# Kernel tuning notes

Measured on AMD Instinct MI355X. Metric: run time of the kernel, lower is better.

## Reference

```python
import jax, jax.numpy as jnp
import numpy as np

GELU = lambda v: jax.nn.gelu(v, approximate=False)  # torch nn.GELU default (exact erf)


def _gconv(x, w):
    # grouped conv1d, valid padding; w: (C,1,K), groups=C. lax conv = cross-correlation, same as torch.
    return jax.lax.conv_general_dilated(x, w, (1,), [(0, 0)],
                                        dimension_numbers=('NCH', 'OIH', 'NCH'),
                                        feature_group_count=x.shape[1])


def _conv(x, w, b):
    # dense conv1d, kernel 3, padding=1
    y = jax.lax.conv_general_dilated(x, w, (1,), [(1, 1)],
                                     dimension_numbers=('NCH', 'OIH', 'NCH'))
    return y + b[None, :, None]


def setup_inputs() -> dict:
    key = jax.random.key(0)
    ks = jax.random.split(key, 12)
    B, C, L = 8, 64, 2048
    H, FL, HD, TD, level = 32, 8, 64, 16, 3
    Cs = (1 + level) * C  # 256 channels into the ODE
    n = lambda k, s: (jax.random.normal(k, s) * 0.05).astype(jnp.float32)
    z = lambda s: jnp.zeros(s, jnp.float32)
    return dict(
        x=jax.random.normal(ks[0], (B, C, L), jnp.float32),
        # DyWAN_QR params
        sw1=n(ks[1], (H, C)), sb1=z((H,)),
        sw2=n(ks[2], (H, H)), sb2=z((H,)),
        sw3=n(ks[3], (2 * FL, H)), sb3=z((2 * FL,)),
        # ODE time embed / FiLM params
        tw1=n(ks[4], (TD, 1)), tb1=z((TD,)),
        tw2=n(ks[5], (TD, TD)), tb2=z((TD,)),
        cw=n(ks[6], (2 * HD, TD)), cb=z((2 * HD,)),
        # ODE conv stack params
        k1=n(ks[7], (HD, Cs, 3)), kb1=z((HD,)),
        k2=n(ks[8], (HD, HD, 3)), kb2=z((HD,)),
        k3=n(ks[9], (Cs, HD, 3)), kb3=z((Cs,)),
    )


def reference(x, sw1, sb1, sw2, sb2, sw3, sb3, tw1, tb1, tw2, tb2, cw, cb,
              k1, kb1, k2, kb2, k3, kb3):
    B, C, L = x.shape
    level, FL, T = 3, 8, 5

    def dywan(a):
        # stat_net: adaptive max pool over L -> (B,C) -> Linear -> GELU
        feat = GELU(jnp.max(a, axis=-1) @ sw1.T + sb1)
        raw = GELU(feat @ sw2.T + sb2) @ sw3.T + sb3  # (B, 2*FL)
        lo_raw, hi_raw = raw[:, :FL], raw[:, FL:]
        # QR of an (FL,1) column vector == L2 normalization (up to LAPACK sign)
        lo = lo_raw / jnp.linalg.norm(lo_raw, axis=1, keepdims=True)
        hi = hi_raw / jnp.linalg.norm(hi_raw, axis=1, keepdims=True)
        return lo, hi

    pad = FL - 1
    coeffs = [x]
    approx = x
    for _ in range(level):
        lo, hi = dywan(approx)
        lo_f = jnp.broadcast_to(lo.mean(0)[None, None, :], (C, 1, FL))
        hi_f = jnp.broadcast_to(hi.mean(0)[None, None, :], (C, 1, FL))
        ap = jnp.pad(approx, ((0, 0), (0, 0), (pad // 2, pad - pad // 2)), mode='reflect')
        new_approx = _gconv(ap, lo_f)[..., :L]
        coeffs.append(_gconv(ap, hi_f)[..., :L])
        approx = new_approx
    stacked = jnp.concatenate(coeffs, axis=1)  # (B, (1+level)*C, L)

    def ode_f(t, y):
        te = jnp.reshape(t, (1, 1)).astype(y.dtype)
        te = GELU(te @ tw1.T + tb1) @ tw2.T + tb2          # (1, TD)
        cond = te @ cw.T + cb                               # (1, 2*HD)
        hd = cond.shape[1] // 2
        gamma, beta = cond[:, :hd], cond[:, hd:]
        h = _conv(y, k1, kb1)
        h = (1.0 + gamma[:, :, None]) * h + beta[:, :, None]  # FiLM
        h = GELU(h)
        h = GELU(_conv(h, k2, kb2))
        return _conv(h, k3, kb3)

    # dopri5 tableau, fixed grid over linspace(0, 1, T) (b7 = 0, so 6 stages)
    hs = 1.0 / (T - 1)
    y = stacked
    for i in range(T - 1):
        t0 = i * hs
        s1 = ode_f(t0, y)
        s2 = ode_f(t0 + hs / 5, y + hs * (1 / 5) * s1)
        s3 = ode_f(t0 + 3 * hs / 10, y + hs * (3 / 40 * s1 + 9 / 40 * s2))
        s4 = ode_f(t0 + 4 * hs / 5, y + hs * (44 / 45 * s1 - 56 / 15 * s2 + 32 / 9 * s3))
        s5 = ode_f(t0 + 8 * hs / 9, y + hs * (19372 / 6561 * s1 - 25360 / 2187 * s2
                                              + 64448 / 6561 * s3 - 212 / 729 * s4))
        s6 = ode_f(t0 + hs, y + hs * (9017 / 3168 * s1 - 355 / 33 * s2 + 46732 / 5247 * s3
                                      + 49 / 176 * s4 - 5103 / 18656 * s5))
        y = y + hs * (35 / 384 * s1 + 500 / 1113 * s3 + 125 / 192 * s4
                      - 2187 / 6784 * s5 + 11 / 84 * s6)
    ode_out = y

    yl = ode_out[:, :C, :]
    yh0 = ode_out[:, C:2 * C, :]
    yh1 = ode_out[:, 2 * C:3 * C, :]
    yh2 = ode_out[:, 3 * C:4 * C, :]

    dx = ode_f(jnp.float32(1.0), ode_out)
    inner = jnp.sum(stacked * dx, axis=(1, 2))  # (B,)
    ecloss = jnp.mean(inner ** 2)
    return (yl, yh0, yh1, yh2, ecloss)
```

## Files before the change

kernel.cpp:

```cpp
#include <hip/hip_runtime.h>
#include <math.h>

#define B 8
#define C 64
#define L 2048
#define CS 256
#define BCL  (B*C*L)
#define BCSL (B*CS*L)
#define HS 0.25f

typedef unsigned short u16;
typedef unsigned int   u32;
typedef __attribute__((ext_vector_type(8))) short sh8;
typedef __attribute__((ext_vector_type(4))) float f4;
typedef __attribute__((ext_vector_type(8))) unsigned short us8;
typedef __attribute__((ext_vector_type(4))) unsigned short us4;

__device__ __forceinline__ float gelu(float x) {
    return 0.5f * x * (1.0f + erff(x * 0.70710678118654752440f));
}
__device__ __forceinline__ u16 f2b(float f) {
    u32 u = __float_as_uint(f);
    u32 r = u + 0x7FFFu + ((u >> 16) & 1u);
    return (u16)(r >> 16);
}
__device__ __forceinline__ float b2f(u16 h) {
    return __uint_as_float(((u32)h) << 16);
}

struct ComboB { const u16* p[6]; float c[6]; };

__global__ __launch_bounds__(256) void prep_k(const float* __restrict__ w,
        u16* __restrict__ dst, int IC, int OC) {
    int idx = blockIdx.x * 256 + threadIdx.x;
    int OCG = OC >> 4;
    int j = idx & 7, lane = (idx >> 3) & 63, t = idx >> 9;
    int ocg = t % OCG, c = t / OCG;
    int oc = ocg * 16 + (lane & 15);
    int K = c * 32 + ((lane >> 4) & 3) * 8 + j;
    int kk = K / IC, ic = K % IC;
    dst[idx] = f2b(w[((size_t)oc * IC + ic) * 3 + kk]);
}

__global__ void cond25_k(const float* __restrict__ tw1, const float* __restrict__ tb1,
                         const float* __restrict__ tw2, const float* __restrict__ tb2,
                         const float* __restrict__ cw, const float* __restrict__ cb,
                         float* __restrict__ condall) {
    __shared__ float te1[16], te2[16];
    int tix = blockIdx.x;
    int tid = threadIdx.x;
    double add[6] = {0.0, 0.25/5.0, 3.0*0.25/10.0, 4.0*0.25/5.0, 8.0*0.25/9.0, 0.25};
    float t = (tix == 24) ? 1.0f : (float)((double)(tix / 6) * 0.25 + add[tix % 6]);
    if (tid < 16) te1[tid] = gelu(t * tw1[tid] + tb1[tid]);
    __syncthreads();
    if (tid < 16) {
        float s = tb2[tid];
        for (int k = 0; k < 16; ++k) s += te1[k] * tw2[tid*16+k];
        te2[tid] = s;
    }
    __syncthreads();
    float s = cb[tid];
    for (int j = 0; j < 16; ++j) s += te2[j] * cw[tid*16+j];
    condall[tix*128 + tid] = s;
}

template<int NC, int EPI>
__global__ __launch_bounds__(256, 8) void fused_k(ComboB in,
        const u16* __restrict__ wp1, const float* __restrict__ kb1,
        const u16* __restrict__ wp2, const float* __restrict__ kb2,
        const u16* __restrict__ wp3, const float* __restrict__ kb3,
        const float* __restrict__ condall, int tix,
        u16* __restrict__ outSb,
        float* __restrict__ ytr, u16* __restrict__ yb,
        float* __restrict__ outp, const float* __restrict__ stacked,
        double* __restrict__ inner)
{
    __shared__ u16 xs1[16][264];
    __shared__ u16 h1t[12][72];
    __shared__ u16 h2t[10][72];
    __shared__ u16 ypart[8][264];
    __shared__ double sred[4];
    const int tid = threadIdx.x;
    const int bx  = blockIdx.x;
    const int tile = ((bx & 7) << 5) | (bx >> 3);
    const int l0  = tile * 8;
    const int b   = blockIdx.y;

    const float cy1 = HS*(35.f/384.f), cy3 = HS*(500.f/1113.f),
                cy4 = HS*(125.f/192.f), cy5 = -HS*(2187.f/6784.f),
                cy6 = HS*(11.f/84.f);

    for (int i = tid; i < 264; i += 256) ((u32*)&xs1[14][0])[i] = 0;

    #pragma unroll
    for (int it = 0; it < 2; ++it) {
        int idx = it * 256 + tid;
        if (idx < 448) {
            int r = idx >> 5, c8 = idx & 31;
            int gl = l0 - 3 + r;
            us8 val;
            if (gl >= 0 && gl < L) {
                size_t a = ((size_t)b * L + gl) * 256 + c8 * 8;
                us8 v0 = *(const us8*)(in.p[0] + a);
                if (NC == 1) {
                    val = v0;
                } else {
                    float f[8], yp[8];
                    #pragma unroll
                    for (int j = 0; j < 8; ++j) { f[j] = b2f(v0[j]); yp[j] = 0.f; }
                    #pragma unroll
                    for (int t = 1; t < NC; ++t) {
                        us8 vt = *(const us8*)(in.p[t] + a);
                        #pragma unroll
                        for (int j = 0; j < 8; ++j) {
                            float bv = b2f(vt[j]);
                            f[j] += in.c[t] * bv;
                            if ((EPI == 1 || EPI == 2) && (t == 1 || t == 3 || t == 4 || t == 5)) {
                                float cy = (t == 1) ? cy1 : (t == 3) ? cy3 : (t == 4) ? cy4 : cy5;
                                yp[j] += cy * bv;
                            }
                        }
                    }
                    #pragma unroll
                    for (int j = 0; j < 8; ++j) val[j] = f2b(f[j]);
                    if ((EPI == 1 || EPI == 2) && r >= 3 && r < 11) {
                        us8 ypk;
                        #pragma unroll
                        for (int j = 0; j < 8; ++j) ypk[j] = f2b(yp[j]);
                        *(us8*)&ypart[r - 3][c8 * 8] = ypk;
                    }
                }
            } else {
                #pragma unroll
                for (int j = 0; j < 8; ++j) val[j] = 0;
            }
            *(us8*)&xs1[r][c8 * 8] = val;
        }
    }
    __syncthreads();

    const int wave = tid >> 6, lane = tid & 63;
    const int nlo = lane & 15, quad = lane >> 4;

    f4 a1 = {0.f,0.f,0.f,0.f};
    {
        const sh8* w1 = (const sh8*)wp1;
        for (int c = 0; c < 24; ++c) {
            int kk = c >> 3, ic0 = (c & 7) << 5;
            sh8 A = w1[(c*4 + wave)*64 + lane];
            int row = nlo + kk; row = row > 15 ? 15 : row;
            sh8 Bv = *(const sh8*)&xs1[row][ic0 + quad*8];
            a1 = __builtin_amdgcn_mfma_f32_16x16x32_bf16(A, Bv, a1, 0, 0, 0);
        }
    }
    {
        const float* cd = condall + tix*128;
        int p = nlo;
        int gp = l0 - 2 + p;
        bool ok = (gp >= 0) && (gp < L);
        if (p < 12) {
            #pragma unroll
            for (int reg = 0; reg < 4; ++reg) {
                int oc = wave*16 + quad*4 + reg;
                float v = (1.f + cd[oc]) * (a1[reg] + kb1[oc]) + cd[64+oc];
                h1t[p][oc] = ok ? f2b(gelu(v)) : (u16)0;
            }
        }
    }
    __syncthreads();

    f4 a2 = {0.f,0.f,0.f,0.f};
    {
        const sh8* w2 = (const sh8*)wp2;
        #pragma unroll
        for (int c = 0; c < 6; ++c) {
            int kk = c >> 1, ic0 = (c & 1) << 5;
            sh8 A = w2[(c*4 + wave)*64 + lane];
            int row = nlo + kk; row = row > 11 ? 11 : row;
            sh8 Bv = *(const sh8*)&h1t[row][ic0 + quad*8];
            a2 = __builtin_amdgcn_mfma_f32_16x16x32_bf16(A, Bv, a2, 0, 0, 0);
        }
    }
    {
        int q = nlo;
        int gq = l0 - 1 + q;
        bool ok = (gq >= 0) && (gq < L);
        if (q < 10) {
            #pragma unroll
            for (int reg = 0; reg < 4; ++reg) {
                int oc = wave*16 + quad*4 + reg;
                h2t[q][oc] = ok ? f2b(gelu(a2[reg] + kb2[oc])) : (u16)0;
            }
        }
    }
    __syncthreads();

    f4 a3[4];
    #pragma unroll
    for (int mf = 0; mf < 4; ++mf) a3[mf] = f4{0.f,0.f,0.f,0.f};
    {
        const sh8* w3 = (const sh8*)wp3;
        #pragma unroll
        for (int c = 0; c < 6; ++c) {
            int kk = c >> 1, ic0 = (c & 1) << 5;
            int row = nlo + kk; row = row > 9 ? 9 : row;
            sh8 B0 = *(const sh8*)&h2t[row][ic0 + quad*8];
            #pragma unroll
            for (int mf = 0; mf < 4; ++mf) {
                sh8 A = w3[(c*16 + wave*4 + mf)*64 + lane];
                a3[mf] = __builtin_amdgcn_mfma_f32_16x16x32_bf16(A, B0, a3[mf], 0, 0, 0);
            }
        }
    }

    const int pos = l0 + nlo;
    if (EPI == 3) {
        double acc = 0.0;
        if (nlo < 8) {
            #pragma unroll
            for (int mf = 0; mf < 4; ++mf)
                #pragma unroll
                for (int reg = 0; reg < 4; ++reg) {
                    int oc = (wave*4 + mf)*16 + quad*4 + reg;
                    size_t idx = ((size_t)b*CS + oc)*L + pos;
                    float dx = a3[mf][reg] + kb3[oc];
                    acc += (double)stacked[idx] * (double)dx;
                }
        }
        #pragma unroll
        for (int off = 32; off > 0; off >>= 1) acc += __shfl_down(acc, off, 64);
        if (lane == 0) sred[wave] = acc;
        __syncthreads();
        if (tid == 0) atomicAdd(&inner[b], sred[0] + sred[1] + sred[2] + sred[3]);
    } else if (EPI == 0) {
        if (nlo < 8) {
            #pragma unroll
            for (int mf = 0; mf < 4; ++mf) {
                int baseoc = (wave*4 + mf)*16 + quad*4;
                us4 pk;
                #pragma unroll
                for (int reg = 0; reg < 4; ++reg)
                    pk[reg] = f2b(a3[mf][reg] + kb3[baseoc + reg]);
                *(us4*)(outSb + ((size_t)b*L + pos)*256 + baseoc) = pk;
            }
        }
    } else {
        if (nlo < 8) {
            #pragma unroll
            for (int mf = 0; mf < 4; ++mf) {
                int baseoc = (wave*4 + mf)*16 + quad*4;
                size_t ta = ((size_t)b*L + pos)*256 + baseoc;
                us4 yp4 = *(const us4*)&ypart[nlo][baseoc];
                f4 y4 = *(const f4*)(ytr + ta);
                us4 pk;
                f4 yo;
                #pragma unroll
                for (int reg = 0; reg < 4; ++reg) {
                    int oc = baseoc + reg;
                    float s6 = a3[mf][reg] + kb3[oc];
                    float yv = y4[reg] + b2f(yp4[reg]) + cy6 * s6;
                    yo[reg] = yv;
                    pk[reg] = f2b(yv);
                    if (EPI == 2) {
                        size_t oidx = (((size_t)(oc >> 6)*B + b)*64 + (oc & 63))*L + pos;
                        outp[oidx] = yv;
                    }
                }
                if (EPI == 1) *(f4*)(ytr + ta) = yo;
                *(us4*)(yb + ta) = pk;
            }
        }
    }
}

__global__ __launch_bounds__(256) void rowmax_k(const float* __restrict__ a, float* __restrict__ bm) {
    __shared__ float red[256];
    int row = blockIdx.x;
    const float* p = a + (size_t)row * L;
    float m = -1e30f;
    for (int t = threadIdx.x; t < L; t += 256) m = fmaxf(m, p[t]);
    red[threadIdx.x] = m;
    __syncthreads();
    for (int s = 128; s > 0; s >>= 1) {
        if (threadIdx.x < s) red[threadIdx.x] = fmaxf(red[threadIdx.x], red[threadIdx.x + s]);
        __syncthreads();
    }
    if (threadIdx.x == 0) bm[row] = red[0];
}

__global__ __launch_bounds__(256) void mlp_k(const float* __restrict__ bm,
    const float* __restrict__ sw1, const float* __restrict__ sb1,
    const float* __restrict__ sw2, const float* __restrict__ sb2,
    const float* __restrict__ sw3, const float* __restrict__ sb3,
    float* __restrict__ filt) {
    __shared__ float m[8][64], f1[8][32], f2[8][32], raw[8][16], nrm[8][2];
    int tid = threadIdx.x;
    for (int i = tid; i < 512; i += 256) m[i >> 6][i & 63] = bm[i];
    __syncthreads();
    {
        int b = tid >> 5, h = tid & 31;
        float s = sb1[h];
        for (int c = 0; c < 64; ++c) s += m[b][c] * sw1[h*64+c];
        f1[b][h] = gelu(s);
    }
    __syncthreads();
    {
        int b = tid >> 5, h = tid & 31;
        float s = sb2[h];
        for (int k = 0; k < 32; ++k) s += f1[b][k] * sw2[h*32+k];
        f2[b][h] = gelu(s);
    }
    __syncthreads();
    if (tid < 128) {
        int b = tid >> 4, j = tid & 15;
        float s = sb3[j];
        for (int k = 0; k < 32; ++k) s += f2[b][k] * sw3[j*32+k];
        raw[b][j] = s;
    }
    __syncthreads();
    if (tid < 16) {
        int b = tid >> 1, half = tid & 1;
        float s = 0.f;
        for (int j = 0; j < 8; ++j) { float v = raw[b][half*8+j]; s += v*v; }
        nrm[b][half] = sqrtf(s);
    }
    __syncthreads();
    if (tid < 16) {
        int half = tid >> 3;
        float s = 0.f;
        for (int b = 0; b < 8; ++b) s += raw[b][tid] / nrm[b][half];
        filt[tid] = s * 0.125f;
    }
}

__global__ __launch_bounds__(256) void wconv_k(const float* __restrict__ ap,
    const float* __restrict__ filt, float* __restrict__ apOut,
    float* __restrict__ stacked, int lev) {
    __shared__ float f[16];
    if (threadIdx.x < 16) f[threadIdx.x] = filt[threadIdx.x];
    __syncthreads();
    size_t idx = (size_t)blockIdx.x * 256 + threadIdx.x;
    int l = (int)(idx & 2047);
    size_t bc = idx >> 11;
    int c = (int)(bc & 63), b = (int)(bc >> 6);
    const float* row = ap + (bc << 11);
    float lo = 0.f, hi = 0.f;
    #pragma unroll
    for (int k = 0; k < 8; ++k) {
        int mI = l + k - 3;
        mI = mI < 0 ? -mI : (mI >= L ? 2*L - 2 - mI : mI);
        float v = row[mI];
        lo += v * f[k];
        hi += v * f[8+k];
    }
    apOut[idx] = lo;
    stacked[((size_t)b * CS + (size_t)(lev+1) * 64 + c) * L + l] = hi;
}

__global__ __launch_bounds__(256) void copyx_k(const float* __restrict__ x, float* __restrict__ st) {
    size_t i = (size_t)blockIdx.x * 256 + threadIdx.x;
    size_t b = i >> 17, rem = i & 131071;
    st[b * ((size_t)CS*L) + rem] = x[i];
}

__global__ __launch_bounds__(256) void tinit_k(const float* __restrict__ st,
        float* __restrict__ ytr, u16* __restrict__ yb) {
    __shared__ float t[64][65];
    const int tid = threadIdx.x;
    const int l0 = blockIdx.x * 64, c0 = blockIdx.y * 64, b = blockIdx.z;
    #pragma unroll
    for (int k = 0; k < 16; ++k) {
        int c = k * 4 + (tid >> 6), l = tid & 63;
        t[c][l] = st[((size_t)b*CS + c0 + c) * L + l0 + l];
    }
    __syncthreads();
    #pragma unroll
    for (int k = 0; k < 16; ++k) {
        int p = k * 4 + (tid >> 6), ch = tid & 63;
        float v = t[ch][p];
        size_t ta = ((size_t)b * L + l0 + p) * 256 + c0 + ch;
        ytr[ta] = v;
        yb[ta] = f2b(v);
    }
}

__global__ void ecfin_k(const double* __restrict__ inner, float* __restrict__ out) {
    double s = 0.0;
    for (int b = 0; b < 8; ++b) s += inner[b] * inner[b];
    out[BCSL] = (float)(s / 8.0);
}

extern "C" void kernel_launch(void* const* d_in, const int* in_sizes, int n_in,
                              void* d_out, int out_size, void* d_ws, size_t ws_size,
                              hipStream_t stream) {
    const float* x   = (const float*)d_in[0];
    const float* sw1 = (const float*)d_in[1];
    const float* sb1 = (const float*)d_in[2];
    const float* sw2 = (const float*)d_in[3];
    const float* sb2 = (const float*)d_in[4];
    const float* sw3 = (const float*)d_in[5];
    const float* sb3 = (const float*)d_in[6];
    const float* tw1 = (const float*)d_in[7];
    const float* tb1 = (const float*)d_in[8];
    const float* tw2 = (const float*)d_in[9];
    const float* tb2 = (const float*)d_in[10];
    const float* cw  = (const float*)d_in[11];
    const float* cb  = (const float*)d_in[12];
    const float* k1  = (const float*)d_in[13];
    const float* kb1 = (const float*)d_in[14];
    const float* k2  = (const float*)d_in[15];
    const float* kb2 = (const float*)d_in[16];
    const float* k3  = (const float*)d_in[17];
    const float* kb3 = (const float*)d_in[18];
    float* out = (float*)d_out;

    char* cur = (char*)d_ws;
    auto alloc = [&](size_t bytes) { void* p = cur; cur += (bytes + 255) & ~(size_t)255; return p; };
    float* stacked = (float*)alloc(BCSL * 4);
    float* ytr     = (float*)alloc(BCSL * 4);
    u16*   yb      = (u16*)  alloc(BCSL * 2);
    u16*   sbuf[5];
    for (int i = 0; i < 5; ++i) sbuf[i] = (u16*)alloc(BCSL * 2);
    float* cond  = (float*)alloc(3200 * 4);
    float* bmax  = (float*)alloc(512 * 4);
    float* filt  = (float*)alloc(16 * 4);
    double* inner = (double*)alloc(8 * 8);
    u16* wp1 = (u16*)alloc(49152 * 2);
    u16* wp2 = (u16*)alloc(12288 * 2);
    u16* wp3 = (u16*)alloc(49152 * 2);

    u16 *s1b = sbuf[0], *s2b = sbuf[1], *s3b = sbuf[2], *s4b = sbuf[3], *s5b = sbuf[4];

    hipMemsetAsync(inner, 0, 8 * sizeof(double), stream);

    prep_k<<<192, 256, 0, stream>>>(k1, wp1, CS, C);
    prep_k<<<48,  256, 0, stream>>>(k2, wp2, C,  C);
    prep_k<<<192, 256, 0, stream>>>(k3, wp3, C,  CS);
    cond25_k<<<25, 128, 0, stream>>>(tw1, tb1, tw2, tb2, cw, cb, cond);

    copyx_k<<<4096, 256, 0, stream>>>(x, stacked);
    const float* apIn = x;
    float* apBuf[2] = {(float*)s1b, (float*)s2b};
    for (int lev = 0; lev < 3; ++lev) {
        rowmax_k<<<512, 256, 0, stream>>>(apIn, bmax);
        mlp_k<<<1, 256, 0, stream>>>(bmax, sw1, sb1, sw2, sb2, sw3, sb3, filt);
        float* apOut = apBuf[lev & 1];
        wconv_k<<<4096, 256, 0, stream>>>(apIn, filt, apOut, stacked, lev);
        apIn = apOut;
    }
    tinit_k<<<dim3(32, 4, 8), 256, 0, stream>>>(stacked, ytr, yb);

    const float hs = HS;
    dim3 cg(256, 8);
    #define LAUNCH(NC, EPI, CIN, TIX, OUTSB, OUTP, STK) \
        fused_k<NC, EPI><<<cg, 256, 0, stream>>>(CIN, wp1, kb1, wp2, kb2, wp3, kb3, \
            cond, TIX, OUTSB, ytr, yb, OUTP, STK, inner)

    for (int i = 0; i < 4; ++i) {
        ComboB cA{}; cA.p[0] = yb;
        LAUNCH(1, 0, cA, i*6+0, s1b, nullptr, nullptr);

        ComboB cB{}; cB.p[0] = yb; cB.p[1] = s1b; cB.c[1] = hs*(1.f/5.f);
        LAUNCH(2, 0, cB, i*6+1, s2b, nullptr, nullptr);

        ComboB cC{}; cC.p[0] = yb;
        cC.p[1] = s1b; cC.c[1] = hs*(3.f/40.f);
        cC.p[2] = s2b; cC.c[2] = hs*(9.f/40.f);
        LAUNCH(3, 0, cC, i*6+2, s3b, nullptr, nullptr);

        ComboB cD{}; cD.p[0] = yb;
        cD.p[1] = s1b; cD.c[1] = hs*(44.f/45.f);
        cD.p[2] = s2b; cD.c[2] = -hs*(56.f/15.f);
        cD.p[3] = s3b; cD.c[3] = hs*(32.f/9.f);
        LAUNCH(4, 0, cD, i*6+3, s4b, nullptr, nullptr);

        ComboB cE{}; cE.p[0] = yb;
        cE.p[1] = s1b; cE.c[1] = hs*(19372.f/6561.f);
        cE.p[2] = s2b; cE.c[2] = -hs*(25360.f/2187.f);
        cE.p[3] = s3b; cE.c[3] = hs*(64448.f/6561.f);
        cE.p[4] = s4b; cE.c[4] = -hs*(212.f/729.f);
        LAUNCH(5, 0, cE, i*6+4, s5b, nullptr, nullptr);

        ComboB cF{}; cF.p[0] = yb;
        cF.p[1] = s1b; cF.c[1] = hs*(9017.f/3168.f);
        cF.p[2] = s2b; cF.c[2] = -hs*(355.f/33.f);
        cF.p[3] = s3b; cF.c[3] = hs*(46732.f/5247.f);
        cF.p[4] = s4b; cF.c[4] = hs*(49.f/176.f);
        cF.p[5] = s5b; cF.c[5] = -hs*(5103.f/18656.f);
        if (i < 3) {
            LAUNCH(6, 1, cF, i*6+5, nullptr, nullptr, nullptr);
        } else {
            LAUNCH(6, 2, cF, i*6+5, nullptr, out, nullptr);
        }
    }

    ComboB cZ{}; cZ.p[0] = yb;
    LAUNCH(1, 3, cZ, 24, nullptr, nullptr, stacked);
    ecfin_k<<<1, 1, 0, stream>>>(inner, out);
    #undef LAUNCH
}
```

Baseline: 782.1 us.

## Fuse all six RK stages into one kernel per step with LDS halo recompute

Replaces the 24 per-stage kernel launches with 4 per-step kernels. Each workgroup loads a 16-position tile plus an 18-position halo of y into LDS, then computes all six Dormand-Prince stages locally, keeping the intermediate stage results in shared memory instead of global bf16 buffers. This removes the global round-trips for s1..s5 and most launch overhead, at the cost of redundant halo compute (52 rows for 16 outputs), large LDS use (~1 workgroup per CU) and fewer blocks. The final dx/ecloss evaluation moves to a separate 16-wide kernel.

Measured after the change: 1.235 ms. +57.9%, slower.

```diff
diff --git a/kernel.cpp b/kernel.cpp
--- a/kernel.cpp
+++ b/kernel.cpp
@@ -27,8 +27,6 @@
 __device__ __forceinline__ float b2f(u16 h) {
     return __uint_as_float(((u32)h) << 16);
 }
-
-struct ComboB { const u16* p[6]; float c[6]; };
 
 __global__ __launch_bounds__(256) void prep_k(const float* __restrict__ w,
         u16* __restrict__ dst, int IC, int OC) {
@@ -64,212 +62,397 @@
     condall[tix*128 + tid] = s;
 }
 
-template<int NC, int EPI>
-__global__ __launch_bounds__(256, 8) void fused_k(ComboB in,
-        const u16* __restrict__ wp1, const float* __restrict__ kb1,
-        const u16* __restrict__ wp2, const float* __restrict__ kb2,
-        const u16* __restrict__ wp3, const float* __restrict__ kb3,
-        const float* __restrict__ condall, int tix,
-        u16* __restrict__ outSb,
-        float* __restrict__ ytr, u16* __restrict__ yb,
-        float* __restrict__ outp, const float* __restrict__ stacked,
-        double* __restrict__ inner)
+
+template<int K, int STEP>
+__device__ __forceinline__ void do_stage(int tid, int l0, int b,
+    const u16* __restrict__ wp1, const float* __restrict__ kb1,
+    const u16* __restrict__ wp2, const float* __restrict__ kb2,
+    const u16* __restrict__ wp3, const float* __restrict__ kb3,
+    const float* __restrict__ condall,
+    u16 (&ybt)[52][264], u16 (&xs)[52][264],
+    u16 (&s1t)[46][264], u16 (&s2t)[40][264], u16 (&s3t)[34][264],
+    u16 (&s4t)[28][264], u16 (&s5t)[22][264],
+    u16 (&h1)[52][72], u16 (&h2)[52][72],
+    float* __restrict__ ytr, u16* __restrict__ ybo, float* __restrict__ outp)
 {
-    __shared__ u16 xs1[16][264];
-    __shared__ u16 h1t[12][72];
-    __shared__ u16 h2t[10][72];
-    __shared__ u16 ypart[8][264];
-    __shared__ double sred[4];
-    const int tid = threadIdx.x;
-    const int bx  = blockIdx.x;
-    const int tile = ((bx & 7) << 5) | (bx >> 3);
-    const int l0  = tile * 8;
-    const int b   = blockIdx.y;
-
-    const float cy1 = HS*(35.f/384.f), cy3 = HS*(500.f/1113.f),
-                cy4 = HS*(125.f/192.f), cy5 = -HS*(2187.f/6784.f),
-                cy6 = HS*(11.f/84.f);
-
-    for (int i = tid; i < 264; i += 256) ((u32*)&xs1[14][0])[i] = 0;
-
-    #pragma unroll
-    for (int it = 0; it < 2; ++it) {
-        int idx = it * 256 + tid;
-        if (idx < 448) {
-            int r = idx >> 5, c8 = idx & 31;
-            int gl = l0 - 3 + r;
-            us8 val;
-            if (gl >= 0 && gl < L) {
-                size_t a = ((size_t)b * L + gl) * 256 + c8 * 8;
-                us8 v0 = *(const us8*)(in.p[0] + a);
-                if (NC == 1) {
-                    val = v0;
-                } else {
-                    float f[8], yp[8];
-                    #pragma unroll
-                    for (int j = 0; j < 8; ++j) { f[j] = b2f(v0[j]); yp[j] = 0.f; }
-                    #pragma unroll
-                    for (int t = 1; t < NC; ++t) {
-                        us8 vt = *(const us8*)(in.p[t] + a);
-                        #pragma unroll
-                        for (int j = 0; j < 8; ++j) {
-                            float bv = b2f(vt[j]);
-                            f[j] += in.c[t] * bv;
-                            if ((EPI == 1 || EPI == 2) && (t == 1 || t == 3 || t == 4 || t == 5)) {
-                                float cy = (t == 1) ? cy1 : (t == 3) ? cy3 : (t == 4) ? cy4 : cy5;
-                                yp[j] += cy * bv;
-                            }
-                        }
-                    }
-                    #pragma unroll
-                    for (int j = 0; j < 8; ++j) val[j] = f2b(f[j]);
-                    if ((EPI == 1 || EPI == 2) && r >= 3 && r < 11) {
-                        us8 ypk;
-                        #pragma unroll
-                        for (int j = 0; j < 8; ++j) ypk[j] = f2b(yp[j]);
-                        *(us8*)&ypart[r - 3][c8 * 8] = ypk;
-                    }
-                }
-            } else {
-                #pragma unroll
-                for (int j = 0; j < 8; ++j) val[j] = 0;
-            }
-            *(us8*)&xs1[r][c8 * 8] = val;
-        }
-    }
-    __syncthreads();
-
+    constexpr int OFF = 3 * K;
+    constexpr int N   = 52 - 6 * K;
+    constexpr int NF1 = (N + 4 + 15) / 16;
+    constexpr int NF2 = (N + 2 + 15) / 16;
+    constexpr int NF3 = (N + 15) / 16;
     const int wave = tid >> 6, lane = tid & 63;
     const int nlo = lane & 15, quad = lane >> 4;
 
-    f4 a1 = {0.f,0.f,0.f,0.f};
-    {
+    if (K >= 2) {
+        const float a1 = HS * (K==2 ? 1.f/5.f : K==3 ? 3.f/40.f : K==4 ? 44.f/45.f :
+                               K==5 ? 19372.f/6561.f : 9017.f/3168.f);
+        const float a2 = HS * (K==3 ? 9.f/40.f : K==4 ? -56.f/15.f :
+                               K==5 ? -25360.f/2187.f : -355.f/33.f);
+        const float a3 = HS * (K==4 ? 32.f/9.f : K==5 ? 64448.f/6561.f : 46732.f/5247.f);
+        const float a4 = HS * (K==5 ? -212.f/729.f : 49.f/176.f);
+        const float a5 = HS * (-5103.f/18656.f);
+        constexpr int rows = N + 6, base = OFF - 3, items = rows * 32;
+        #pragma unroll
+        for (int it = 0; it < (items + 255) / 256; ++it) {
+            int idx = it * 256 + tid;
+            if (idx < items) {
+                int r = base + (idx >> 5), co = (idx & 31) * 8;
+                float f[8];
+                us8 v = *(const us8*)&ybt[r][co];
+                #pragma unroll
+                for (int j = 0; j < 8; ++j) f[j] = b2f(v[j]);
+                { us8 w = *(const us8*)&s1t[r-3][co];
+                  #pragma unroll
+                  for (int j = 0; j < 8; ++j) f[j] += a1 * b2f(w[j]); }
+                if (K >= 3) { us8 w = *(const us8*)&s2t[r-6][co];
+                  #pragma unroll
+                  for (int j = 0; j < 8; ++j) f[j] += a2 * b2f(w[j]); }
+                if (K >= 4) { us8 w = *(const us8*)&s3t[r-9][co];
+                  #pragma unroll
+                  for (int j = 0; j < 8; ++j) f[j] += a3 * b2f(w[j]); }
+                if (K >= 5) { us8 w = *(const us8*)&s4t[r-12][co];
+                  #pragma unroll
+                  for (int j = 0; j < 8; ++j) f[j] += a4 * b2f(w[j]); }
+                if (K >= 6) { us8 w = *(const us8*)&s5t[r-15][co];
+                  #pragma unroll
+                  for (int j = 0; j < 8; ++j) f[j] += a5 * b2f(w[j]); }
+                us8 o;
+                #pragma unroll
+                for (int j = 0; j < 8; ++j) o[j] = f2b(f[j]);
+                *(us8*)&xs[r][co] = o;
+            }
+        }
+        __syncthreads();
+    }
+    u16 (&xq)[52][264] = (K == 1) ? ybt : xs;
+
+    {
+        f4 acc[NF1];
+        #pragma unroll
+        for (int j = 0; j < NF1; ++j) acc[j] = f4{0.f,0.f,0.f,0.f};
         const sh8* w1 = (const sh8*)wp1;
         for (int c = 0; c < 24; ++c) {
             int kk = c >> 3, ic0 = (c & 7) << 5;
             sh8 A = w1[(c*4 + wave)*64 + lane];
-            int row = nlo + kk; row = row > 15 ? 15 : row;
-            sh8 Bv = *(const sh8*)&xs1[row][ic0 + quad*8];
-            a1 = __builtin_amdgcn_mfma_f32_16x16x32_bf16(A, Bv, a1, 0, 0, 0);
-        }
-    }
-    {
-        const float* cd = condall + tix*128;
-        int p = nlo;
-        int gp = l0 - 2 + p;
-        bool ok = (gp >= 0) && (gp < L);
-        if (p < 12) {
-            #pragma unroll
-            for (int reg = 0; reg < 4; ++reg) {
-                int oc = wave*16 + quad*4 + reg;
-                float v = (1.f + cd[oc]) * (a1[reg] + kb1[oc]) + cd[64+oc];
-                h1t[p][oc] = ok ? f2b(gelu(v)) : (u16)0;
-            }
-        }
-    }
-    __syncthreads();
-
-    f4 a2 = {0.f,0.f,0.f,0.f};
-    {
+            #pragma unroll
+            for (int j = 0; j < NF1; ++j) {
+                int row = OFF - 3 + 16*j + nlo + kk;
+                row = row > 51 ? 51 : row;
+                sh8 Bv = *(const sh8*)&xq[row][ic0 + quad*8];
+                acc[j] = __builtin_amdgcn_mfma_f32_16x16x32_bf16(A, Bv, acc[j], 0, 0, 0);
+            }
+        }
+        const float* cd = condall + (STEP*6 + (K-1))*128;
+        #pragma unroll
+        for (int j = 0; j < NF1; ++j) {
+            int p = OFF - 2 + 16*j + nlo;
+            if (p < 52) {
+                int gp = l0 - 18 + p;
+                bool ok = (p < OFF + N + 2) && (gp >= 0) && (gp < L);
+                #pragma unroll
+                for (int reg = 0; reg < 4; ++reg) {
+                    int oc = wave*16 + quad*4 + reg;
+                    float v = (1.f + cd[oc]) * (acc[j][reg] + kb1[oc]) + cd[64+oc];
+                    h1[p][oc] = ok ? f2b(gelu(v)) : (u16)0;
+                }
+            }
+        }
+    }
+    __syncthreads();
+
+    {
+        f4 acc[NF2];
+        #pragma unroll
+        for (int j = 0; j < NF2; ++j) acc[j] = f4{0.f,0.f,0.f,0.f};
         const sh8* w2 = (const sh8*)wp2;
         #pragma unroll
         for (int c = 0; c < 6; ++c) {
             int kk = c >> 1, ic0 = (c & 1) << 5;
             sh8 A = w2[(c*4 + wave)*64 + lane];
-            int row = nlo + kk; row = row > 11 ? 11 : row;
-            sh8 Bv = *(const sh8*)&h1t[row][ic0 + quad*8];
-            a2 = __builtin_amdgcn_mfma_f32_16x16x32_bf16(A, Bv, a2, 0, 0, 0);
-        }
-    }
-    {
-        int q = nlo;
-        int gq = l0 - 1 + q;
-        bool ok = (gq >= 0) && (gq < L);
-        if (q < 10) {
-            #pragma unroll
-            for (int reg = 0; reg < 4; ++reg) {
-                int oc = wave*16 + quad*4 + reg;
-                h2t[q][oc] = ok ? f2b(gelu(a2[reg] + kb2[oc])) : (u16)0;
-            }
-        }
-    }
-    __syncthreads();
-
-    f4 a3[4];
+            #pragma unroll
+            for (int j = 0; j < NF2; ++j) {
+                int row = OFF - 2 + 16*j + nlo + kk;
+                row = row > 51 ? 51 : row;
+                sh8 Bv = *(const sh8*)&h1[row][ic0 + quad*8];
+                acc[j] = __builtin_amdgcn_mfma_f32_16x16x32_bf16(A, Bv, acc[j], 0, 0, 0);
+            }
+        }
+        #pragma unroll
+        for (int j = 0; j < NF2; ++j) {
+            int q = OFF - 1 + 16*j + nlo;
+            if (q < 52) {
+                int gq = l0 - 18 + q;
+                bool ok = (q < OFF + N + 1) && (gq >= 0) && (gq < L);
+                #pragma unroll
+                for (int reg = 0; reg < 4; ++reg) {
+                    int oc = wave*16 + quad*4 + reg;
+                    h2[q][oc] = ok ? f2b(gelu(acc[j][reg] + kb2[oc])) : (u16)0;
+                }
+            }
+        }
+    }
+    __syncthreads();
+
+    f4 acc[NF3][4];
     #pragma unroll
-    for (int mf = 0; mf < 4; ++mf) a3[mf] = f4{0.f,0.f,0.f,0.f};
+    for (int j = 0; j < NF3; ++j)
+        #pragma unroll
+        for (int mf = 0; mf < 4; ++mf) acc[j][mf] = f4{0.f,0.f,0.f,0.f};
     {
         const sh8* w3 = (const sh8*)wp3;
         #pragma unroll
         for (int c = 0; c < 6; ++c) {
             int kk = c >> 1, ic0 = (c & 1) << 5;
-            int row = nlo + kk; row = row > 9 ? 9 : row;
-            sh8 B0 = *(const sh8*)&h2t[row][ic0 + quad*8];
+            #pragma unroll
+            for (int j = 0; j < NF3; ++j) {
+                int row = OFF - 1 + 16*j + nlo + kk;
+                row = row > 51 ? 51 : row;
+                sh8 Bv = *(const sh8*)&h2[row][ic0 + quad*8];
+                #pragma unroll
+                for (int mf = 0; mf < 4; ++mf) {
+                    sh8 A = w3[(c*16 + wave*4 + mf)*64 + lane];
+                    acc[j][mf] = __builtin_amdgcn_mfma_f32_16x16x32_bf16(A, Bv, acc[j][mf], 0, 0, 0);
+                }
+            }
+        }
+    }
+
+    if (K < 6) {
+        #pragma unroll
+        for (int j = 0; j < NF3; ++j) {
+            int p = OFF + 16*j + nlo;
+            if (p < OFF + N) {
+                int gp = l0 - 18 + p;
+                bool ok = (gp >= 0) && (gp < L);
+                #pragma unroll
+                for (int mf = 0; mf < 4; ++mf) {
+                    int baseoc = (wave*4 + mf)*16 + quad*4;
+                    us4 pk;
+                    #pragma unroll
+                    for (int reg = 0; reg < 4; ++reg) {
+                        float v = acc[j][mf][reg] + kb3[baseoc + reg];
+                        pk[reg] = ok ? f2b(v) : (u16)0;
+                    }
+                    if (K == 1) *(us4*)&s1t[p-OFF][baseoc] = pk;
+                    if (K == 2) *(us4*)&s2t[p-OFF][baseoc] = pk;
+                    if (K == 3) *(us4*)&s3t[p-OFF][baseoc] = pk;
+                    if (K == 4) *(us4*)&s4t[p-OFF][baseoc] = pk;
+                    if (K == 5) *(us4*)&s5t[p-OFF][baseoc] = pk;
+                }
+            }
+        }
+        __syncthreads();
+    } else {
+        const float cy1 = HS*(35.f/384.f), cy3 = HS*(500.f/1113.f),
+                    cy4 = HS*(125.f/192.f), cy5 = -HS*(2187.f/6784.f),
+                    cy6 = HS*(11.f/84.f);
+        int p = 18 + nlo;
+        int gp = l0 + nlo;
+        #pragma unroll
+        for (int mf = 0; mf < 4; ++mf) {
+            int baseoc = (wave*4 + mf)*16 + quad*4;
+            size_t ta = ((size_t)b * L + gp) * 256 + baseoc;
+            us4 v1 = *(const us4*)&s1t[p-3][baseoc];
+            us4 v3 = *(const us4*)&s3t[p-9][baseoc];
+            us4 v4 = *(const us4*)&s4t[p-12][baseoc];
+            us4 v5 = *(const us4*)&s5t[p-15][baseoc];
+            f4 y4 = *(const f4*)(ytr + ta);
+            us4 pk; f4 yo;
+            #pragma unroll
+            for (int reg = 0; reg < 4; ++reg) {
+                int oc = baseoc + reg;
+                float s6 = acc[0][mf][reg] + kb3[oc];
+                float yv = y4[reg] + cy1*b2f(v1[reg]) + cy3*b2f(v3[reg])
+                         + cy4*b2f(v4[reg]) + cy5*b2f(v5[reg]) + cy6*s6;
+                yo[reg] = yv;
+                pk[reg] = f2b(yv);
+                if (STEP == 3) {
+                    outp[(((size_t)(oc >> 6)*B + b)*64 + (oc & 63))*L + gp] = yv;
+                }
+            }
+            if (STEP < 3) *(f4*)(ytr + ta) = yo;
+            *(us4*)(ybo + ta) = pk;
+        }
+    }
+}
+
+template<int STEP>
+__global__ __launch_bounds__(256, 1) void rkstep_k(
+    const u16* __restrict__ wp1, const float* __restrict__ kb1,
+    const u16* __restrict__ wp2, const float* __restrict__ kb2,
+    const u16* __restrict__ wp3, const float* __restrict__ kb3,
+    const float* __restrict__ condall,
+    float* __restrict__ ytr, const u16* __restrict__ ybi,
+    u16* __restrict__ ybo, float* __restrict__ outp)
+{
+    __shared__ u16 ybt[52][264], xs[52][264];
+    __shared__ u16 s1t[46][264], s2t[40][264], s3t[34][264], s4t[28][264], s5t[22][264];
+    __shared__ u16 h1[52][72], h2[52][72];
+    const int tid = threadIdx.x;
+    const int bx = blockIdx.x;
+    const int tile = ((bx & 7) << 4) | (bx >> 3);
+    const int l0 = tile * 16;
+    const int b = blockIdx.y;
+
+    #pragma unroll
+    for (int it = 0; it < 7; ++it) {
+        int idx = it * 256 + tid;
+        if (idx < 52 * 32) {
+            int r = idx >> 5, co = (idx & 31) * 8;
+            int gl = l0 - 18 + r;
+            us8 v = {};
+            if (gl >= 0 && gl < L) v = *(const us8*)(ybi + ((size_t)b*L + gl)*256 + co);
+            *(us8*)&ybt[r][co] = v;
+        }
+    }
+    __syncthreads();
+
+    do_stage<1,STEP>(tid, l0, b, wp1,kb1,wp2,kb2,wp3,kb3, condall,
+                     ybt, xs, s1t,s2t,s3t,s4t,s5t, h1,h2, ytr, ybo, outp);
+    do_stage<2,STEP>(tid, l0, b, wp1,kb1,wp2,kb2,wp3,kb3, condall,
+                     ybt, xs, s1t,s2t,s3t,s4t,s5t, h1,h2, ytr, ybo, outp);
+    do_stage<3,STEP>(tid, l0, b, wp1,kb1,wp2,kb2,wp3,kb3, condall,
+                     ybt, xs, s1t,s2t,s3t,s4t,s5t, h1,h2, ytr, ybo, outp);
+    do_stage<4,STEP>(tid, l0, b, wp1,kb1,wp2,kb2,wp3,kb3, condall,
+                     ybt, xs, s1t,s2t,s3t,s4t,s5t, h1,h2, ytr, ybo, outp);
+    do_stage<5,STEP>(tid, l0, b, wp1,kb1,wp2,kb2,wp3,kb3, condall,
+                     ybt, xs, s1t,s2t,s3t,s4t,s5t, h1,h2, ytr, ybo, outp);
+    do_stage<6,STEP>(tid, l0, b, wp1,kb1,wp2,kb2,wp3,kb3, condall,
+                     ybt, xs, s1t,s2t,s3t,s4t,s5t, h1,h2, ytr, ybo, outp);
+}
+
+__global__ __launch_bounds__(256) void dxec_k(
+    const u16* __restrict__ ybi,
+    const u16* __restrict__ wp1, const float* __restrict__ kb1,
+    const u16* __restrict__ wp2, const float* __restrict__ kb2,
+    const u16* __restrict__ wp3, const float* __restrict__ kb3,
+    const float* __restrict__ condall,
+    const float* __restrict__ stacked, double* __restrict__ inner)
+{
+    __shared__ u16 xs[22][264];
+    __shared__ u16 h1[22][72];
+    __shared__ u16 h2[20][72];
+    __shared__ double sred[4];
+    const int tid = threadIdx.x;
+    const int bx = blockIdx.x;
+    const int tile = ((bx & 7) << 4) | (bx >> 3);
+    const int l0 = tile * 16;
+    const int b = blockIdx.y;
+
+    #pragma unroll
+    for (int it = 0; it < 3; ++it) {
+        int idx = it * 256 + tid;
+        if (idx < 22 * 32) {
+            int r = idx >> 5, co = (idx & 31) * 8;
+            int gl = l0 - 3 + r;
+            us8 v = {};
+            if (gl >= 0 && gl < L) v = *(const us8*)(ybi + ((size_t)b*L + gl)*256 + co);
+            *(us8*)&xs[r][co] = v;
+        }
+    }
+    __syncthreads();
+
+    const int wave = tid >> 6, lane = tid & 63;
+    const int nlo = lane & 15, quad = lane >> 4;
+
+    {
+        f4 acc[2];
+        acc[0] = f4{0.f,0.f,0.f,0.f}; acc[1] = acc[0];
+        const sh8* w1 = (const sh8*)wp1;
+        for (int c = 0; c < 24; ++c) {
+            int kk = c >> 3, ic0 = (c & 7) << 5;
+            sh8 A = w1[(c*4 + wave)*64 + lane];
+            #pragma unroll
+            for (int j = 0; j < 2; ++j) {
+                int row = 16*j + nlo + kk;
+                row = row > 21 ? 21 : row;
+                sh8 Bv = *(const sh8*)&xs[row][ic0 + quad*8];
+                acc[j] = __builtin_amdgcn_mfma_f32_16x16x32_bf16(A, Bv, acc[j], 0, 0, 0);
+            }
+        }
+        const float* cd = condall + 24*128;
+        #pragma unroll
+        for (int j = 0; j < 2; ++j) {
+            int p = 1 + 16*j + nlo;
+            if (p < 22) {
+                int gp = l0 - 3 + p;
+                bool ok = (p < 21) && (gp >= 0) && (gp < L);
+                #pragma unroll
+                for (int reg = 0; reg < 4; ++reg) {
+                    int oc = wave*16 + quad*4 + reg;
+                    float v = (1.f + cd[oc]) * (acc[j][reg] + kb1[oc]) + cd[64+oc];
+                    h1[p][oc] = ok ? f2b(gelu(v)) : (u16)0;
+                }
+            }
+        }
+    }
+    __syncthreads();
+
+    {
+        f4 acc[2];
+        acc[0] = f4{0.f,0.f,0.f,0.f}; acc[1] = acc[0];
+        const sh8* w2 = (const sh8*)wp2;
+        #pragma unroll
+        for (int c = 0; c < 6; ++c) {
+            int kk = c >> 1, ic0 = (c & 1) << 5;
+            sh8 A = w2[(c*4 + wave)*64 + lane];
+            #pragma unroll
+            for (int j = 0; j < 2; ++j) {
+                int row = 1 + 16*j + nlo + kk;
+                row = row > 21 ? 21 : row;
+                sh8 Bv = *(const sh8*)&h1[row][ic0 + quad*8];
+                acc[j] = __builtin_amdgcn_mfma_f32_16x16x32_bf16(A, Bv, acc[j], 0, 0, 0);
+            }
+        }
+        #pragma unroll
+        for (int j = 0; j < 2; ++j) {
+            int q = 2 + 16*j + nlo;
+            if (q < 20) {
+                int gq = l0 - 3 + q;
+                bool ok = (gq >= 0) && (gq < L);
+                #pragma unroll
+                for (int reg = 0; reg < 4; ++reg) {
+                    int oc = wave*16 + quad*4 + reg;
+                    h2[q][oc] = ok ? f2b(gelu(acc[j][reg] + kb2[oc])) : (u16)0;
+                }
+            }
+        }
+    }
+    __syncthreads();
+
+    f4 acc[4];
+    #pragma unroll
+    for (int mf = 0; mf < 4; ++mf) acc[mf] = f4{0.f,0.f,0.f,0.f};
+    {
+        const sh8* w3 = (const sh8*)wp3;
+        #pragma unroll
+        for (int c = 0; c < 6; ++c) {
+            int kk = c >> 1, ic0 = (c & 1) << 5;
+            int row = 2 + nlo + kk;
+            sh8 Bv = *(const sh8*)&h2[row][ic0 + quad*8];
             #pragma unroll
             for (int mf = 0; mf < 4; ++mf) {
                 sh8 A = w3[(c*16 + wave*4 + mf)*64 + lane];
-                a3[mf] = __builtin_amdgcn_mfma_f32_16x16x32_bf16(A, B0, a3[mf], 0, 0, 0);
-            }
-        }
-    }
-
-    const int pos = l0 + nlo;
-    if (EPI == 3) {
-        double acc = 0.0;
-        if (nlo < 8) {
-            #pragma unroll
-            for (int mf = 0; mf < 4; ++mf)
-                #pragma unroll
-                for (int reg = 0; reg < 4; ++reg) {
-                    int oc = (wave*4 + mf)*16 + quad*4 + reg;
-                    size_t idx = ((size_t)b*CS + oc)*L + pos;
-                    float dx = a3[mf][reg] + kb3[oc];
-                    acc += (double)stacked[idx] * (double)dx;
-                }
-        }
-        #pragma unroll
-        for (int off = 32; off > 0; off >>= 1) acc += __shfl_down(acc, off, 64);
-        if (lane == 0) sred[wave] = acc;
+                acc[mf] = __builtin_amdgcn_mfma_f32_16x16x32_bf16(A, Bv, acc[mf], 0, 0, 0);
+            }
+        }
+    }
+    {
+        int gp = l0 + nlo;
+        double s = 0.0;
+        #pragma unroll
+        for (int mf = 0; mf < 4; ++mf)
+            #pragma unroll
+            for (int reg = 0; reg < 4; ++reg) {
+                int oc = (wave*4 + mf)*16 + quad*4 + reg;
+                float dx = acc[mf][reg] + kb3[oc];
+                s += (double)stacked[((size_t)b*CS + oc)*L + gp] * (double)dx;
+            }
+        #pragma unroll
+        for (int off = 32; off > 0; off >>= 1) s += __shfl_down(s, off, 64);
+        if (lane == 0) sred[wave] = s;
         __syncthreads();
         if (tid == 0) atomicAdd(&inner[b], sred[0] + sred[1] + sred[2] + sred[3]);
-    } else if (EPI == 0) {
-        if (nlo < 8) {
-            #pragma unroll
-            for (int mf = 0; mf < 4; ++mf) {
-                int baseoc = (wave*4 + mf)*16 + quad*4;
-                us4 pk;
-                #pragma unroll
-                for (int reg = 0; reg < 4; ++reg)
-                    pk[reg] = f2b(a3[mf][reg] + kb3[baseoc + reg]);
-                *(us4*)(outSb + ((size_t)b*L + pos)*256 + baseoc) = pk;
-            }
-        }
-    } else {
-        if (nlo < 8) {
-            #pragma unroll
-            for (int mf = 0; mf < 4; ++mf) {
-                int baseoc = (wave*4 + mf)*16 + quad*4;
-                size_t ta = ((size_t)b*L + pos)*256 + baseoc;
-                us4 yp4 = *(const us4*)&ypart[nlo][baseoc];
-                f4 y4 = *(const f4*)(ytr + ta);
-                us4 pk;
-                f4 yo;
-                #pragma unroll
-                for (int reg = 0; reg < 4; ++reg) {
-                    int oc = baseoc + reg;
-                    float s6 = a3[mf][reg] + kb3[oc];
-                    float yv = y4[reg] + b2f(yp4[reg]) + cy6 * s6;
-                    yo[reg] = yv;
-                    pk[reg] = f2b(yv);
-                    if (EPI == 2) {
-                        size_t oidx = (((size_t)(oc >> 6)*B + b)*64 + (oc & 63))*L + pos;
-                        outp[oidx] = yv;
-                    }
-                }
-                if (EPI == 1) *(f4*)(ytr + ta) = yo;
-                *(us4*)(yb + ta) = pk;
-            }
-        }
     }
 }
 
@@ -418,9 +601,10 @@
     auto alloc = [&](size_t bytes) { void* p = cur; cur += (bytes + 255) & ~(size_t)255; return p; };
     float* stacked = (float*)alloc(BCSL * 4);
     float* ytr     = (float*)alloc(BCSL * 4);
-    u16*   yb      = (u16*)  alloc(BCSL * 2);
-    u16*   sbuf[5];
-    for (int i = 0; i < 5; ++i) sbuf[i] = (u16*)alloc(BCSL * 2);
+    u16*   yb0     = (u16*)  alloc(BCSL * 2);
+    u16*   yb1     = (u16*)  alloc(BCSL * 2);
+    float* wsA     = (float*)alloc(BCL * 4);
+    float* wsB     = (float*)alloc(BCL * 4);
     float* cond  = (float*)alloc(3200 * 4);
     float* bmax  = (float*)alloc(512 * 4);
     float* filt  = (float*)alloc(16 * 4);
@@ -429,8 +613,6 @@
     u16* wp2 = (u16*)alloc(12288 * 2);
     u16* wp3 = (u16*)alloc(49152 * 2);
 
-    u16 *s1b = sbuf[0], *s2b = sbuf[1], *s3b = sbuf[2], *s4b = sbuf[3], *s5b = sbuf[4];
-
     hipMemsetAsync(inner, 0, 8 * sizeof(double), stream);
 
     prep_k<<<192, 256, 0, stream>>>(k1, wp1, CS, C);
@@ -440,7 +622,7 @@
 
     copyx_k<<<4096, 256, 0, stream>>>(x, stacked);
     const float* apIn = x;
-    float* apBuf[2] = {(float*)s1b, (float*)s2b};
+    float* apBuf[2] = {wsA, wsB};
     for (int lev = 0; lev < 3; ++lev) {
         rowmax_k<<<512, 256, 0, stream>>>(apIn, bmax);
         mlp_k<<<1, 256, 0, stream>>>(bmax, sw1, sb1, sw2, sb2, sw3, sb3, filt);
@@ -448,54 +630,19 @@
         wconv_k<<<4096, 256, 0, stream>>>(apIn, filt, apOut, stacked, lev);
         apIn = apOut;
     }
-    tinit_k<<<dim3(32, 4, 8), 256, 0, stream>>>(stacked, ytr, yb);
-
-    const float hs = HS;
-    dim3 cg(256, 8);
-    #define LAUNCH(NC, EPI, CIN, TIX, OUTSB, OUTP, STK) \
-        fused_k<NC, EPI><<<cg, 256, 0, stream>>>(CIN, wp1, kb1, wp2, kb2, wp3, kb3, \
-            cond, TIX, OUTSB, ytr, yb, OUTP, STK, inner)
-
-    for (int i = 0; i < 4; ++i) {
-        ComboB cA{}; cA.p[0] = yb;
-        LAUNCH(1, 0, cA, i*6+0, s1b, nullptr, nullptr);
-
-        ComboB cB{}; cB.p[0] = yb; cB.p[1] = s1b; cB.c[1] = hs*(1.f/5.f);
-        LAUNCH(2, 0, cB, i*6+1, s2b, nullptr, nullptr);
-
-        ComboB cC{}; cC.p[0] = yb;
-        cC.p[1] = s1b; cC.c[1] = hs*(3.f/40.f);
-        cC.p[2] = s2b; cC.c[2] = hs*(9.f/40.f);
-        LAUNCH(3, 0, cC, i*6+2, s3b, nullptr, nullptr);
-
-        ComboB cD{}; cD.p[0] = yb;
-        cD.p[1] = s1b; cD.c[1] = hs*(44.f/45.f);
-        cD.p[2] = s2b; cD.c[2] = -hs*(56.f/15.f);
-        cD.p[3] = s3b; cD.c[3] = hs*(32.f/9.f);
-        LAUNCH(4, 0, cD, i*6+3, s4b, nullptr, nullptr);
-
-        ComboB cE{}; cE.p[0] = yb;
-        cE.p[1] = s1b; cE.c[1] = hs*(19372.f/6561.f);
-        cE.p[2] = s2b; cE.c[2] = -hs*(25360.f/2187.f);
-        cE.p[3] = s3b; cE.c[3] = hs*(64448.f/6561.f);
-        cE.p[4] = s4b; cE.c[4] = -hs*(212.f/729.f);
-        LAUNCH(5, 0, cE, i*6+4, s5b, nullptr, nullptr);
-
-        ComboB cF{}; cF.p[0] = yb;
-        cF.p[1] = s1b; cF.c[1] = hs*(9017.f/3168.f);
-        cF.p[2] = s2b; cF.c[2] = -hs*(355.f/33.f);
-        cF.p[3] = s3b; cF.c[3] = hs*(46732.f/5247.f);
-        cF.p[4] = s4b; cF.c[4] = hs*(49.f/176.f);
-        cF.p[5] = s5b; cF.c[5] = -hs*(5103.f/18656.f);
-        if (i < 3) {
-            LAUNCH(6, 1, cF, i*6+5, nullptr, nullptr, nullptr);
-        } else {
-            LAUNCH(6, 2, cF, i*6+5, nullptr, out, nullptr);
-        }
-    }
-
-    ComboB cZ{}; cZ.p[0] = yb;
-    LAUNCH(1, 3, cZ, 24, nullptr, nullptr, stacked);
+    tinit_k<<<dim3(32, 4, 8), 256, 0, stream>>>(stacked, ytr, yb0);
+
+    dim3 cg(128, 8);
+    rkstep_k<0><<<cg, 256, 0, stream>>>(wp1, kb1, wp2, kb2, wp3, kb3, cond,
+                                        ytr, yb0, yb1, nullptr);
+    rkstep_k<1><<<cg, 256, 0, stream>>>(wp1, kb1, wp2, kb2, wp3, kb3, cond,
+                                        ytr, yb1, yb0, nullptr);
+    rkstep_k<2><<<cg, 256, 0, stream>>>(wp1, kb1, wp2, kb2, wp3, kb3, cond,
+                                        ytr, yb0, yb1, nullptr);
+    rkstep_k<3><<<cg, 256, 0, stream>>>(wp1, kb1, wp2, kb2, wp3, kb3, cond,
+                                        ytr, yb1, yb0, out);
+
+    dxec_k<<<cg, 256, 0, stream>>>(yb0, wp1, kb1, wp2, kb2, wp3, kb3, cond,
+                                   stacked, inner);
     ecfin_k<<<1, 1, 0, stream>>>(inner, out);
-    #undef LAUNCH
-}
+}
```
